# Optimization experiments

Measured on AMD Instinct MI355X. Metric: run time of the kernel, lower is better.

## Reference

```python
import jax, jax.numpy as jnp
import numpy as np

B, S, D, H = 4, 2048, 1024, 16
HD = D // H
NEG = -1e30


def setup_inputs() -> dict:
    key = jax.random.key(0)
    ks = jax.random.split(key, 6)
    scale = 1.0 / np.sqrt(D)
    return {
        "q": jax.random.normal(ks[0], (B, S, D), jnp.float32),
        "k": jax.random.normal(ks[1], (B, S, D), jnp.float32),
        "v": jax.random.normal(ks[2], (B, S, D), jnp.float32),
        "mask": jnp.ones((B, 1, S), jnp.float32),
        "wq": jax.random.normal(ks[3], (D, D), jnp.float32) * scale,
        "bq": jnp.zeros((D,), jnp.float32),
        "wk": jax.random.normal(ks[4], (D, D), jnp.float32) * scale,
        "bk": jnp.zeros((D,), jnp.float32),
        "wv": jax.random.normal(ks[5], (D, D), jnp.float32) * scale,
        "bv": jnp.zeros((D,), jnp.float32),
    }


def _heads(x):
    # (B,S,D) -> (B,H,S,HD)
    return x.reshape(B, S, H, HD).transpose(0, 2, 1, 3)


def reference(q, k, v, mask, wq, bq, wk, bk, wv, bv):
    # pointwise Conv1D(kernel=1) == linear: x @ W^T + b (W: (out,in))
    qh = _heads(jnp.einsum('bsd,ed->bse', q, wq) + bq)
    kh = _heads(jnp.einsum('bsd,ed->bse', k, wk) + bk)
    vh = _heads(jnp.einsum('bsd,ed->bse', v, wv) + bv)
    scores = jnp.einsum('bhqd,bhkd->bhqk', qh, kh) / jnp.sqrt(jnp.float32(HD))
    # mask_logits: x + (1 - mask) * -1e30, mask (B,1,S) -> (B,1,1,S)
    scores = scores + (1.0 - mask[:, None, :, :]) * NEG
    probs = jax.nn.softmax(scores, axis=-1)  # dropout is identity in eval
    ctx = jnp.einsum('bhqk,bhkd->bhqd', probs, vh)
    return ctx.transpose(0, 2, 1, 3).reshape(B, S, D)
```

## Files before the change

### kernel.cpp

```cpp
#include <hip/hip_runtime.h>
#include <math.h>

typedef __attribute__((ext_vector_type(8)))  _Float16 f16x8;
typedef __attribute__((ext_vector_type(4)))  _Float16 f16x4;
typedef __attribute__((ext_vector_type(2)))  __fp16   h16x2;
typedef __attribute__((ext_vector_type(4)))  float    f32x4;
typedef __attribute__((ext_vector_type(16))) float    f32x16;
typedef unsigned int u32;

static constexpr int B  = 4;
static constexpr int S  = 2048;
static constexpr int D  = 1024;
static constexpr int H  = 16;
static constexpr int HD = 64;

union U64cvt { f16x4 h; ushort4 u; };
union W4 { u32 w[4]; f16x8 v; };

__device__ __forceinline__ void gld16(const void* g, void* l) {
    __builtin_amdgcn_global_load_lds((const u32*)g, (u32*)l, 16, 0, 0);
}

__device__ __forceinline__ void cvtwr16(const float4& x, const float4& y, void* dst) {
    W4 w;
    w.w[0] = __builtin_bit_cast(u32, __builtin_amdgcn_cvt_pkrtz(x.x, x.y));
    w.w[1] = __builtin_bit_cast(u32, __builtin_amdgcn_cvt_pkrtz(x.z, x.w));
    w.w[2] = __builtin_bit_cast(u32, __builtin_amdgcn_cvt_pkrtz(y.x, y.y));
    w.w[3] = __builtin_bit_cast(u32, __builtin_amdgcn_cvt_pkrtz(y.z, y.w));
    *(f16x8*)dst = w.v;
}

__global__ __launch_bounds__(256)
void cvt_prep(const float* __restrict__ q, const float* __restrict__ k,
              const float* __restrict__ v,
              const float* __restrict__ wq, const float* __restrict__ wk,
              const float* __restrict__ wv,
              unsigned short* __restrict__ dst)
{
    const int c = blockIdx.x * 256 + threadIdx.x;
    const float* src;
    size_t idx;
    if (c < 3145728) {
        const int a = c >> 20;
        src = (a == 0) ? q : (a == 1) ? k : v;
        idx = (size_t)(c & 1048575) * 8;
    } else {
        const int c2 = c - 3145728;
        const int a = c2 >> 17;
        src = (a == 0) ? wq : (a == 1) ? wk : wv;
        idx = (size_t)(c2 & 131071) * 8;
    }
    const float4 x = *(const float4*)(src + idx);
    const float4 y = *(const float4*)(src + idx + 4);
    cvtwr16(x, y, dst + (size_t)c * 8);
}

__global__ __launch_bounds__(256)
void proj_f16(const unsigned short* __restrict__ af16,
              const unsigned short* __restrict__ wf16,
              const float* __restrict__ bqp, const float* __restrict__ bkp,
              const float* __restrict__ bvp,
              unsigned short* __restrict__ outs)
{
    const int bid = blockIdx.x;
    const int xcd = bid & 7;
    const int idx = bid >> 3;
    const int z   = idx / 64;
    const int r2  = idx - z * 64;
    const int mpl = r2 >> 3;
    const int np  = r2 & 7;
    const int mp  = (xcd >> 1) * 16 + (xcd & 1) * 8 + mpl;
    const int m0  = mp * 128;
    const int n0  = np * 128;

    const unsigned short* A  = af16 + (size_t)z * 8388608;
    const unsigned short* Wf = wf16 + (size_t)z * 1048576;
    const float* bias = (z == 0) ? bqp : (z == 1) ? bkp : bvp;
    unsigned short* out = outs + (size_t)z * 8388608;

    const int tid  = threadIdx.x;
    const int lane = tid & 63;
    const int wid  = tid >> 6;
    const int wr   = wid >> 1;
    const int wc   = wid & 1;

    __shared__ __align__(16) unsigned char lA[2][8192];
    __shared__ __align__(16) unsigned char lB[2][8192];

    f32x4 acc[4][4];
#pragma unroll
    for (int i = 0; i < 4; ++i)
#pragma unroll
        for (int j = 0; j < 4; ++j) acc[i][j] = (f32x4){0.f, 0.f, 0.f, 0.f};

    int grow[2], gcol[2], lbase[2];
#pragma unroll
    for (int i = 0; i < 2; ++i) {
        const int c = tid + 256 * i;
        grow[i]  = c >> 2;
        gcol[i]  = ((c & 3) - (grow[i] >> 1)) & 3;
        lbase[i] = (c & ~63) * 16;
    }

#pragma unroll
    for (int i = 0; i < 2; ++i) {
        gld16(A  + (size_t)(m0 + grow[i]) * D + gcol[i] * 8, lA[0] + lbase[i]);
        gld16(Wf + (size_t)(n0 + grow[i]) * D + gcol[i] * 8, lB[0] + lbase[i]);
    }
    __syncthreads();

    for (int kt = 0; kt < 32; ++kt) {
        const int cb = kt & 1, nx = cb ^ 1;

        if (kt < 31) {
            const int k1 = (kt + 1) * 32;
#pragma unroll
            for (int i = 0; i < 2; ++i) {
                gld16(A  + (size_t)(m0 + grow[i]) * D + k1 + gcol[i] * 8, lA[nx] + lbase[i]);
                gld16(Wf + (size_t)(n0 + grow[i]) * D + k1 + gcol[i] * 8, lB[nx] + lbase[i]);
            }
        }

        f16x8 af[4], bf[4];
#pragma unroll
        for (int mi = 0; mi < 4; ++mi) {
            const int row = wr * 64 + mi * 16 + (lane & 15);
            const int cc  = ((lane >> 4) + (row >> 1)) & 3;
            af[mi] = *(const f16x8*)(lA[cb] + row * 64 + cc * 16);
        }
#pragma unroll
        for (int ni = 0; ni < 4; ++ni) {
            const int row = wc * 64 + ni * 16 + (lane & 15);
            const int cc  = ((lane >> 4) + (row >> 1)) & 3;
            bf[ni] = *(const f16x8*)(lB[cb] + row * 64 + cc * 16);
        }

        __builtin_amdgcn_s_setprio(1);
#pragma unroll
        for (int mi = 0; mi < 4; ++mi)
#pragma unroll
            for (int ni = 0; ni < 4; ++ni)
                acc[mi][ni] = __builtin_amdgcn_mfma_f32_16x16x32_f16(af[mi], bf[ni], acc[mi][ni], 0, 0, 0);
        __builtin_amdgcn_s_setprio(0);

        __syncthreads();
    }

#pragma unroll
    for (int mi = 0; mi < 4; ++mi) {
        const int gmBase = m0 + wr * 64 + mi * 16 + ((lane >> 4) << 2);
        const int b  = gmBase >> 11;
        const int s0 = gmBase & 2047;
        const int tV   = s0 >> 6;
        const int kv6  = s0 & 63;
        const int ksg  = kv6 >> 4;
        const int hi2v = (kv6 >> 3) & 1;
        const int jb   = kv6 & 7;
#pragma unroll
        for (int ni = 0; ni < 4; ++ni) {
            const int gn = n0 + wc * 64 + ni * 16 + (lane & 15);
            const float bb = bias[gn];
            const int hh = gn >> 6;
            const int hd = gn & 63;
            const size_t bhbase = ((size_t)b * H + hh) * ((size_t)S * HD);
            if (z == 0) {
#pragma unroll
                for (int r = 0; r < 4; ++r) {
                    const int gm = gmBase + r;
                    const _Float16 hv = (_Float16)(acc[mi][ni][r] + bb);
                    out[bhbase + (size_t)(gm & 2047) * HD + hd] =
                        __builtin_bit_cast(unsigned short, hv);
                }
            } else if (z == 1) {
                const int ks   = hd >> 4;
                const int hi2k = (hd >> 3) & 1;
                const int j    = hd & 7;
#pragma unroll
                for (int r = 0; r < 4; ++r) {
                    const int s = (gmBase + r) & 2047;
                    const int t = s >> 6;
                    const int q = ((s >> 5) & 1) * 4 + ks;
                    const _Float16 hv = (_Float16)(acc[mi][ni][r] + bb);
                    out[bhbase + (((size_t)t * 8 + q) * 64 + hi2k * 32 + (s & 31)) * 8 + j] =
                        __builtin_bit_cast(unsigned short, hv);
                }
            } else {
                const int nb  = hd >> 5;
                const int c31 = hd & 31;
                const int q   = nb * 4 + ksg;
                U64cvt uu;
#pragma unroll
                for (int r = 0; r < 4; ++r)
                    uu.h[r] = (_Float16)(acc[mi][ni][r] + bb);
                *(ushort4*)(out + bhbase +
                    (((size_t)tV * 8 + q) * 64 + hi2v * 32 + c31) * 8 + jb) = uu.u;
            }
        }
    }
}

__global__ __launch_bounds__(256)
void proj_qkv(const float* __restrict__ qi, const float* __restrict__ ki,
              const float* __restrict__ vi,
              const float* __restrict__ wqp, const float* __restrict__ wkp,
              const float* __restrict__ wvp,
              const float* __restrict__ bqp, const float* __restrict__ bkp,
              const float* __restrict__ bvp,
              unsigned short* __restrict__ ws)
{
    const int bid = blockIdx.x;
    const int xcd = bid & 7;
    const int idx = bid >> 3;
    const int z   = idx / 64;
    const int r2  = idx - z * 64;
    const int mpl = r2 >> 3;
    const int np  = r2 & 7;
    const int mp  = (xcd >> 1) * 16 + (xcd & 1) * 8 + mpl;
    const int m0  = mp * 128;
    const int n0  = np * 128;

    const float* A    = (z == 0) ? qi  : (z == 1) ? ki  : vi;
    const float* W    = (z == 0) ? wqp : (z == 1) ? wkp : wvp;
    const float* bias = (z == 0) ? bqp : (z == 1) ? bkp : bvp;
    unsigned short* out = ws + (size_t)z * ((size_t)B * S * D);

    const int tid  = threadIdx.x;
    const int lane = tid & 63;
    const int wid  = tid >> 6;
    const int wr   = wid >> 1;
    const int wc   = wid & 1;

    __shared__ __align__(16) unsigned char lA[2][8192];
    __shared__ __align__(16) unsigned char lB[2][8192];

    f32x4 acc[4][4];
#pragma unroll
    for (int i = 0; i < 4; ++i)
#pragma unroll
        for (int j = 0; j < 4; ++j) acc[i][j] = (f32x4){0.f, 0.f, 0.f, 0.f};

    const int rb = (lane >> 4) * 16;

    int srow[2], sc8[2], soff[2];
#pragma unroll
    for (int i = 0; i < 2; ++i) {
        const int f = tid + 256 * i;
        srow[i] = f >> 2;
        sc8[i]  = f & 3;
        soff[i] = ((f >> 2) * 64 + (f & 3) * 16) ^ ((((f >> 2)) & 7) << 4);
    }

#pragma unroll
    for (int i = 0; i < 2; ++i) {
        const float* pa = A + (size_t)(m0 + srow[i]) * D + sc8[i] * 8;
        const float* pw = W + (size_t)(n0 + srow[i]) * D + sc8[i] * 8;
        cvtwr16(*(const float4*)pa, *(const float4*)(pa + 4), lA[0] + soff[i]);
        cvtwr16(*(const float4*)pw, *(const float4*)(pw + 4), lB[0] + soff[i]);
    }
    float4 pa0[2], pa1[2], pw0[2], pw1[2];
#pragma unroll
    for (int i = 0; i < 2; ++i) {
        const float* pa = A + (size_t)(m0 + srow[i]) * D + 32 + sc8[i] * 8;
        const float* pw = W + (size_t)(n0 + srow[i]) * D + 32 + sc8[i] * 8;
        pa0[i] = *(const float4*)pa;  pa1[i] = *(const float4*)(pa + 4);
        pw0[i] = *(const float4*)pw;  pw1[i] = *(const float4*)(pw + 4);
    }
    __syncthreads();

    for (int kt = 0; kt < 32; ++kt) {
        const int cb = kt & 1, nx = cb ^ 1;
        if (kt < 31) {
#pragma unroll
            for (int i = 0; i < 2; ++i) {
                cvtwr16(pa0[i], pa1[i], lA[nx] + soff[i]);
                cvtwr16(pw0[i], pw1[i], lB[nx] + soff[i]);
            }
        }
        f16x8 af[4], bf[4];
#pragma unroll
        for (int mi = 0; mi < 4; ++mi) {
            const int row = wr * 64 + mi * 16 + (lane & 15);
            af[mi] = *(const f16x8*)(lA[cb] + ((row * 64 + rb) ^ ((row & 7) << 4)));
        }
#pragma unroll
        for (int ni = 0; ni < 4; ++ni) {
            const int row = wc * 64 + ni * 16 + (lane & 15);
            bf[ni] = *(const f16x8*)(lB[cb] + ((row * 64 + rb) ^ ((row & 7) << 4)));
        }
        if (kt < 30) {
            const int k2 = (kt + 2) * 32;
#pragma unroll
            for (int i = 0; i < 2; ++i) {
                const float* pa = A + (size_t)(m0 + srow[i]) * D + k2 + sc8[i] * 8;
                const float* pw = W + (size_t)(n0 + srow[i]) * D + k2 + sc8[i] * 8;
                pa0[i] = *(const float4*)pa;  pa1[i] = *(const float4*)(pa + 4);
                pw0[i] = *(const float4*)pw;  pw1[i] = *(const float4*)(pw + 4);
            }
        }
        __builtin_amdgcn_s_setprio(1);
#pragma unroll
        for (int mi = 0; mi < 4; ++mi)
#pragma unroll
            for (int ni = 0; ni < 4; ++ni)
                acc[mi][ni] = __builtin_amdgcn_mfma_f32_16x16x32_f16(af[mi], bf[ni], acc[mi][ni], 0, 0, 0);
        __builtin_amdgcn_s_setprio(0);
        __syncthreads();
    }

#pragma unroll
    for (int mi = 0; mi < 4; ++mi) {
        const int gmBase = m0 + wr * 64 + mi * 16 + ((lane >> 4) << 2);
        const int b  = gmBase >> 11;
        const int s0 = gmBase & 2047;
        const int tV   = s0 >> 6;
        const int kv6  = s0 & 63;
        const int ksg  = kv6 >> 4;
        const int hi2v = (kv6 >> 3) & 1;
        const int jb   = kv6 & 7;
#pragma unroll
        for (int ni = 0; ni < 4; ++ni) {
            const int gn = n0 + wc * 64 + ni * 16 + (lane & 15);
            const float bb = bias[gn];
            const int hh = gn >> 6;
            const int hd = gn & 63;
            const size_t bhbase = ((size_t)b * H + hh) * ((size_t)S * HD);
            if (z == 0) {
#pragma unroll
                for (int r = 0; r < 4; ++r) {
                    const int gm = gmBase + r;
                    const _Float16 hv = (_Float16)(acc[mi][ni][r] + bb);
                    out[bhbase + (size_t)(gm & 2047) * HD + hd] =
                        __builtin_bit_cast(unsigned short, hv);
                }
            } else if (z == 1) {
                const int ks   = hd >> 4;
                const int hi2k = (hd >> 3) & 1;
                const int j    = hd & 7;
#pragma unroll
                for (int r = 0; r < 4; ++r) {
                    const int s = (gmBase + r) & 2047;
                    const int t = s >> 6;
                    const int q = ((s >> 5) & 1) * 4 + ks;
                    const _Float16 hv = (_Float16)(acc[mi][ni][r] + bb);
                    out[bhbase + (((size_t)t * 8 + q) * 64 + hi2k * 32 + (s & 31)) * 8 + j] =
                        __builtin_bit_cast(unsigned short, hv);
                }
            } else {
                const int nb  = hd >> 5;
                const int c31 = hd & 31;
                const int q   = nb * 4 + ksg;
                U64cvt uu;
#pragma unroll
                for (int r = 0; r < 4; ++r)
                    uu.h[r] = (_Float16)(acc[mi][ni][r] + bb);
                *(ushort4*)(out + bhbase +
                    (((size_t)tV * 8 + q) * 64 + hi2v * 32 + c31) * 8 + jb) = uu.u;
            }
        }
    }
}

__global__ __launch_bounds__(256)
void attn_f16(const unsigned short* __restrict__ qh,
              const unsigned short* __restrict__ kf,
              const unsigned short* __restrict__ vf,
              const float* __restrict__ mask,
              float* __restrict__ out)
{
    const int flat = blockIdx.y * gridDim.x + blockIdx.x;
    const int sw   = (flat & 7) * 128 + (flat >> 3);
    const int bh   = sw >> 4;
    const int q0   = (sw & 15) * 128;

    const int b = bh >> 4;
    const int h = bh & 15;
    const unsigned short* Q  = qh + (size_t)bh * S * HD;
    const unsigned short* KF = kf + (size_t)bh * S * HD;
    const unsigned short* VF = vf + (size_t)bh * S * HD;

    const int tid  = threadIdx.x;
    const int lane = tid & 63;
    const int wid  = tid >> 6;
    const int l31  = lane & 31;
    const int hi2  = lane >> 5;

    __shared__ __align__(16) unsigned char Kl[3][8192];
    __shared__ __align__(16) unsigned char Vl[3][8192];
    __shared__ __align__(16) float maskall[2048];

    const int ldsA = wid * 1024;
    const int ldsB = wid * 1024 + 4096;
    const int g0   = tid * 8;
    const int g1   = tid * 8 + 2048;

    const float C = 0.18033688011112042f;
    const float SHIFT = -5.770780163555854f;

    f16x8 aq[4];
    {
        const unsigned short* qrow = Q + (size_t)(q0 + wid * 32 + l31) * HD;
#pragma unroll
        for (int ks = 0; ks < 4; ++ks)
            aq[ks] = *(const f16x8*)(qrow + ks * 16 + hi2 * 8);
    }

    float ls0 = 0.f, ls1 = 0.f;
    f32x16 accO[2];
    accO[0] = (f32x16){};
    accO[1] = (f32x16){};
    const h16x2 one2 = {(__fp16)1.0f, (__fp16)1.0f};

    {
        const float* mrow = mask + (size_t)b * S + tid * 8;
        const float4 mv0 = *(const float4*)mrow;
        const float4 mv1 = *(const float4*)(mrow + 4);
        f32x4 t0, t1;
        t0[0] = fmaf(1.0f - mv0.x, -1.4426950408889634e30f, SHIFT);
        t0[1] = fmaf(1.0f - mv0.y, -1.4426950408889634e30f, SHIFT);
        t0[2] = fmaf(1.0f - mv0.z, -1.4426950408889634e30f, SHIFT);
        t0[3] = fmaf(1.0f - mv0.w, -1.4426950408889634e30f, SHIFT);
        t1[0] = fmaf(1.0f - mv1.x, -1.4426950408889634e30f, SHIFT);
        t1[1] = fmaf(1.0f - mv1.y, -1.4426950408889634e30f, SHIFT);
        t1[2] = fmaf(1.0f - mv1.z, -1.4426950408889634e30f, SHIFT);
        t1[3] = fmaf(1.0f - mv1.w, -1.4426950408889634e30f, SHIFT);
        *(f32x4*)(maskall + tid * 8)     = t0;
        *(f32x4*)(maskall + tid * 8 + 4) = t1;
    }
    gld16(KF + g0, Kl[0] + ldsA);
    gld16(KF + g1, Kl[0] + ldsB);
    gld16(VF + g0, Vl[0] + ldsA);
    gld16(VF + g1, Vl[0] + ldsB);
    gld16(KF + 4096 + g0, Kl[1] + ldsA);
    gld16(KF + 4096 + g1, Kl[1] + ldsB);
    gld16(VF + 4096 + g0, Vl[1] + ldsA);
    gld16(VF + 4096 + g1, Vl[1] + ldsB);
    __syncthreads();

    const int lane16 = lane * 16;
    int bi = 0;
    for (int t = 0; t < 32; ++t) {
        if (t < 31) {
            asm volatile("s_waitcnt vmcnt(4)" ::: "memory");
        } else {
            asm volatile("s_waitcnt vmcnt(0)" ::: "memory");
        }
        __builtin_amdgcn_s_barrier();
        __builtin_amdgcn_sched_barrier(0);

        if (t < 30) {
            const int b2 = (bi >= 1) ? bi - 1 : bi + 2;
            const size_t nt = (size_t)(t + 2) * 4096;
            gld16(KF + nt + g0, Kl[b2] + ldsA);
            gld16(KF + nt + g1, Kl[b2] + ldsB);
            gld16(VF + nt + g0, Vl[b2] + ldsA);
            gld16(VF + nt + g1, Vl[b2] + ldsB);
        }

        const unsigned char* Kc = Kl[bi];
        const unsigned char* Vc = Vl[bi];

        f32x16 p[2];
        p[0] = (f32x16){};
        p[1] = (f32x16){};
        __builtin_amdgcn_s_setprio(1);
#pragma unroll
        for (int kb = 0; kb < 2; ++kb)
#pragma unroll
            for (int ks = 0; ks < 4; ++ks) {
                const f16x8 ak = *(const f16x8*)(Kc + lane16 + (kb * 4 + ks) * 1024);
                p[kb] = __builtin_amdgcn_mfma_f32_32x32x16_f16(ak, aq[ks], p[kb], 0, 0, 0);
            }
        __builtin_amdgcn_s_setprio(0);

        const float* mt = maskall + t * 64;
        f16x8 pa[4];
#pragma unroll
        for (int kb = 0; kb < 2; ++kb) {
            float pe[16];
#pragma unroll
            for (int g = 0; g < 4; ++g) {
                const f32x4 mg = *(const f32x4*)(mt + kb * 32 + g * 8 + hi2 * 4);
#pragma unroll
                for (int e = 0; e < 4; ++e)
                    pe[g * 4 + e] = exp2f(fmaf(p[kb][g * 4 + e], C, mg[e]));
            }
#pragma unroll
            for (int ks2 = 0; ks2 < 2; ++ks2) {
                const int o = ks2 * 8;
                const h16x2 h0 = __builtin_amdgcn_cvt_pkrtz(pe[o + 0], pe[o + 1]);
                const h16x2 h1 = __builtin_amdgcn_cvt_pkrtz(pe[o + 2], pe[o + 3]);
                const h16x2 h2 = __builtin_amdgcn_cvt_pkrtz(pe[o + 4], pe[o + 5]);
                const h16x2 h3 = __builtin_amdgcn_cvt_pkrtz(pe[o + 6], pe[o + 7]);
                ls0 = __builtin_amdgcn_fdot2(h0, one2, ls0, false);
                ls1 = __builtin_amdgcn_fdot2(h1, one2, ls1, false);
                ls0 = __builtin_amdgcn_fdot2(h2, one2, ls0, false);
                ls1 = __builtin_amdgcn_fdot2(h3, one2, ls1, false);
                u32 a0 = __builtin_bit_cast(u32, h0);
                u32 a1 = __builtin_bit_cast(u32, h1);
                u32 a2 = __builtin_bit_cast(u32, h2);
                u32 a3 = __builtin_bit_cast(u32, h3);
                asm volatile("v_permlane32_swap_b32 %0, %1" : "+v"(a0), "+v"(a2));
                asm volatile("v_permlane32_swap_b32 %0, %1" : "+v"(a1), "+v"(a3));
                W4 w;
                w.w[0] = a0; w.w[1] = a1; w.w[2] = a2; w.w[3] = a3;
                pa[kb * 2 + ks2] = w.v;
            }
        }

        __builtin_amdgcn_s_setprio(1);
#pragma unroll
        for (int nb = 0; nb < 2; ++nb)
#pragma unroll
            for (int ksg = 0; ksg < 4; ++ksg) {
                const f16x8 bv = *(const f16x8*)(Vc + lane16 + (nb * 4 + ksg) * 1024);
                accO[nb] = __builtin_amdgcn_mfma_f32_32x32x16_f16(pa[ksg], bv, accO[nb], 0, 0, 0);
            }
        __builtin_amdgcn_s_setprio(0);

        bi = (bi == 2) ? 0 : bi + 1;
    }

    float lsum = ls0 + ls1;
    lsum += __shfl_xor(lsum, 32);
    const float linv = 1.0f / lsum;

    float lr[16];
#pragma unroll
    for (int r = 0; r < 16; ++r)
        lr[r] = __shfl(linv, (r & 3) + 8 * (r >> 2) + 4 * hi2);

#pragma unroll
    for (int nb = 0; nb < 2; ++nb) {
        const int dcol = h * HD + nb * 32 + l31;
#pragma unroll
        for (int r = 0; r < 16; ++r) {
            const int qrow = q0 + wid * 32 + (r & 3) + 8 * (r >> 2) + 4 * hi2;
            out[((size_t)b * S + qrow) * D + dcol] = accO[nb][r] * lr[r];
        }
    }
}

extern "C" void kernel_launch(void* const* d_in, const int* in_sizes, int n_in,
                              void* d_out, int out_size, void* d_ws, size_t ws_size,
                              hipStream_t stream)
{
    const float* q    = (const float*)d_in[0];
    const float* k    = (const float*)d_in[1];
    const float* v    = (const float*)d_in[2];
    const float* mask = (const float*)d_in[3];
    const float* wq   = (const float*)d_in[4];
    const float* bq   = (const float*)d_in[5];
    const float* wk   = (const float*)d_in[6];
    const float* bk   = (const float*)d_in[7];
    const float* wv   = (const float*)d_in[8];
    const float* bv   = (const float*)d_in[9];

    unsigned short* ws = (unsigned short*)d_ws;
    const size_t per  = (size_t)B * S * D;
    const size_t wsz  = 1048576;
    const size_t need = (3 * per + 3 * wsz + 3 * per) * 2;

    dim3 ga(S / 128, B * H);
    if (ws_size >= need) {
        unsigned short* af16 = ws;
        unsigned short* wf16 = ws + 3 * per;
        unsigned short* outs = ws + 3 * per + 3 * wsz;
        cvt_prep<<<13824, 256, 0, stream>>>(q, k, v, wq, wk, wv, af16);
        proj_f16<<<1536, 256, 0, stream>>>(af16, wf16, bq, bk, bv, outs);
        attn_f16<<<ga, 256, 0, stream>>>(outs, outs + per, outs + 2 * per, mask, (float*)d_out);
    } else {
        proj_qkv<<<1536, 256, 0, stream>>>(q, k, v, wq, wk, wv, bq, bk, bv, ws);
        attn_f16<<<ga, 256, 0, stream>>>(ws, ws + per, ws + 2 * per, mask, (float*)d_out);
    }
}
```

Before: 228.0 us.

## Read K/V fragments directly from global memory instead of LDS triple-buffer

```diff
diff --git a/kernel.cpp b/kernel.cpp
--- a/kernel.cpp
+++ b/kernel.cpp
@@ -384,14 +384,7 @@
     const int l31  = lane & 31;
     const int hi2  = lane >> 5;
 
-    __shared__ __align__(16) unsigned char Kl[3][8192];
-    __shared__ __align__(16) unsigned char Vl[3][8192];
     __shared__ __align__(16) float maskall[2048];
-
-    const int ldsA = wid * 1024;
-    const int ldsB = wid * 1024 + 4096;
-    const int g0   = tid * 8;
-    const int g1   = tid * 8 + 2048;
 
     const float C = 0.18033688011112042f;
     const float SHIFT = -5.770780163555854f;
@@ -426,38 +419,12 @@
         *(f32x4*)(maskall + tid * 8)     = t0;
         *(f32x4*)(maskall + tid * 8 + 4) = t1;
     }
-    gld16(KF + g0, Kl[0] + ldsA);
-    gld16(KF + g1, Kl[0] + ldsB);
-    gld16(VF + g0, Vl[0] + ldsA);
-    gld16(VF + g1, Vl[0] + ldsB);
-    gld16(KF + 4096 + g0, Kl[1] + ldsA);
-    gld16(KF + 4096 + g1, Kl[1] + ldsB);
-    gld16(VF + 4096 + g0, Vl[1] + ldsA);
-    gld16(VF + 4096 + g1, Vl[1] + ldsB);
     __syncthreads();
 
-    const int lane16 = lane * 16;
-    int bi = 0;
+    const int le8 = lane * 8;
     for (int t = 0; t < 32; ++t) {
-        if (t < 31) {
-            asm volatile("s_waitcnt vmcnt(4)" ::: "memory");
-        } else {
-            asm volatile("s_waitcnt vmcnt(0)" ::: "memory");
-        }
-        __builtin_amdgcn_s_barrier();
-        __builtin_amdgcn_sched_barrier(0);
-
-        if (t < 30) {
-            const int b2 = (bi >= 1) ? bi - 1 : bi + 2;
-            const size_t nt = (size_t)(t + 2) * 4096;
-            gld16(KF + nt + g0, Kl[b2] + ldsA);
-            gld16(KF + nt + g1, Kl[b2] + ldsB);
-            gld16(VF + nt + g0, Vl[b2] + ldsA);
-            gld16(VF + nt + g1, Vl[b2] + ldsB);
-        }
-
-        const unsigned char* Kc = Kl[bi];
-        const unsigned char* Vc = Vl[bi];
+        const unsigned short* Kt = KF + t * 4096;
+        const unsigned short* Vt = VF + t * 4096;
 
         f32x16 p[2];
         p[0] = (f32x16){};
@@ -467,7 +434,7 @@
         for (int kb = 0; kb < 2; ++kb)
 #pragma unroll
             for (int ks = 0; ks < 4; ++ks) {
-                const f16x8 ak = *(const f16x8*)(Kc + lane16 + (kb * 4 + ks) * 1024);
+                const f16x8 ak = *(const f16x8*)(Kt + (kb * 4 + ks) * 512 + le8);
                 p[kb] = __builtin_amdgcn_mfma_f32_32x32x16_f16(ak, aq[ks], p[kb], 0, 0, 0);
             }
         __builtin_amdgcn_s_setprio(0);
@@ -512,12 +479,10 @@
         for (int nb = 0; nb < 2; ++nb)
 #pragma unroll
             for (int ksg = 0; ksg < 4; ++ksg) {
-                const f16x8 bv = *(const f16x8*)(Vc + lane16 + (nb * 4 + ksg) * 1024);
+                const f16x8 bv = *(const f16x8*)(Vt + (nb * 4 + ksg) * 512 + le8);
                 accO[nb] = __builtin_amdgcn_mfma_f32_32x32x16_f16(pa[ksg], bv, accO[nb], 0, 0, 0);
             }
         __builtin_amdgcn_s_setprio(0);
-
-        bi = (bi == 2) ? 0 : bi + 1;
     }
 
     float lsum = ls0 + ls1;
```

After: 333.1 us. 46.1% more time.
